# Kernel optimization log

Measured on AMD Instinct MI355X. Metric: run time of the kernel, lower is better.

## Reference

```python
import jax, jax.numpy as jnp
import numpy as np

NEG_POS_RATIO = 3
LOC_LOSS_ALPHA = 1.0
B, N, C = 64, 8732, 21  # batch, total prior boxes (SSD300), classes (VOC)


def setup_inputs() -> dict:
    key = jax.random.key(0)
    kd, km, kl, kpd, kpl = jax.random.split(key, 5)
    pos_mask = jax.random.bernoulli(km, 0.02, (B, N))
    actual_bbox_deltas = jax.random.normal(kd, (B, N, 4), dtype=jnp.float32) * pos_mask[..., None]
    cls = jax.random.randint(kl, (B, N), 0, C)
    actual_labels = jax.nn.one_hot(cls, C, dtype=jnp.float32)
    pred_bbox_deltas = jax.random.normal(kpd, (B, N, 4), dtype=jnp.float32)
    pred_labels = jax.random.normal(kpl, (B, N, C), dtype=jnp.float32)
    return {
        "actual_bbox_deltas": actual_bbox_deltas,
        "actual_labels": actual_labels,
        "pred_bbox_deltas": pred_bbox_deltas,
        "pred_labels": pred_labels,
    }


def reference(actual_bbox_deltas, actual_labels, pred_bbox_deltas, pred_labels):
    # positive boxes: any nonzero delta
    pos_cond = jnp.any(actual_bbox_deltas != 0, axis=2)          # [B, N] bool
    pos_count = jnp.sum(pos_cond, axis=1)                         # [B]
    neg_count = pos_count * NEG_POS_RATIO                         # [B]

    # CE from logits, used only to rank negatives for hard-negative mining
    ce_logits = -jnp.sum(actual_labels * jax.nn.log_softmax(pred_labels, axis=-1), axis=-1)  # [B, N]
    masked_loss = jnp.where(pos_cond, -jnp.inf, ce_logits)
    # rank[b, n] = position of box n in descending sort of masked_loss[b]
    order = jnp.argsort(-masked_loss, axis=1)
    rank = jnp.argsort(order, axis=1)
    neg_mask = rank < neg_count[:, None]                          # hardest negatives
    sel_mask = pos_cond | neg_mask                                # boxes entering conf loss

    total_pos = jnp.maximum(jnp.sum(pos_count), 1).astype(jnp.float32)

    # Huber (delta=1): TF Huber takes mean over last axis, then reduction='sum'
    d = pred_bbox_deltas - actual_bbox_deltas
    ad = jnp.abs(d)
    hub = jnp.where(ad <= 1.0, 0.5 * d * d, ad - 0.5)             # [B, N, 4]
    loc_loss = jnp.sum(jnp.mean(hub, axis=-1) * pos_cond) * LOC_LOSS_ALPHA

    # conf loss: TF CategoricalCrossentropy with from_logits=False (as in the original code,
    # applied to the raw pred_labels): normalize to sum 1, clip to epsilon, -sum(y*log p)
    eps = 1e-7
    p = pred_labels / jnp.sum(pred_labels, axis=-1, keepdims=True)
    p = jnp.clip(p, eps, 1.0 - eps)
    ce_probs = -jnp.sum(actual_labels * jnp.log(p), axis=-1)      # [B, N]
    conf_loss = jnp.sum(ce_probs * sel_mask)

    return loc_loss / total_pos, conf_loss / total_pos
```

## Files before the change

### kernel.cpp

```cpp
#include <hip/hip_runtime.h>
#include <math.h>

#define BB 64
#define NN 8732
#define NV4 (NN / 4)
#define CC 21
#define TB 128
#define GX 69
#define NIT 6

typedef unsigned int u32;
typedef __attribute__((address_space(1))) const u32 gu32;
typedef __attribute__((address_space(3))) u32 lu32;

static __device__ __forceinline__ unsigned f2u(float f) {
  unsigned u = __float_as_uint(f);
  return (u & 0x80000000u) ? ~u : (u | 0x80000000u);
}

__global__ __launch_bounds__(128) void k1_map(
    const float* __restrict__ abd, const float* __restrict__ lbl,
    const float* __restrict__ pbd, const float* __restrict__ plog,
    unsigned* __restrict__ keys, float* __restrict__ cep,
    float* __restrict__ pl, float* __restrict__ pc, int* __restrict__ pcnt) {
  __shared__ __align__(16) float s_plog[TB * CC];
  __shared__ int s_cls[TB];
  __shared__ float s_l[2], s_p[2];
  __shared__ int s_c[2];

  const int b = blockIdx.y;
  const int base = blockIdx.x * TB;
  const int nbox = min(TB, NN - base);
  const int nf4 = (nbox * CC) >> 2;
  const int tid = threadIdx.x;
  const int lane = tid & 63, wv = tid >> 6;

  const float4* pl4 = reinterpret_cast<const float4*>(plog + ((size_t)b * NN + base) * CC);
#pragma unroll
  for (int it = 0; it < NIT; ++it) {
    const int t = it * TB + tid;
    if (t < nf4) {
      __builtin_amdgcn_global_load_lds(
          (gu32*)(const u32*)(pl4 + t),
          (lu32*)(u32*)((char*)s_plog + (size_t)(it * TB + (tid & 64)) * 16),
          16, 0, 0);
    }
  }

  const float4* lb4 = reinterpret_cast<const float4*>(lbl + ((size_t)b * NN + base) * CC);
  float4 lv4[NIT];
#pragma unroll
  for (int it = 0; it < NIT; ++it) {
    const int t = it * TB + tid;
    lv4[it] = lb4[(t < nf4) ? t : 0];
  }
  const int nclamp = base + ((tid < nbox) ? tid : 0);
  const size_t idxc = (size_t)b * NN + nclamp;
  const float4 a = reinterpret_cast<const float4*>(abd)[idxc];
  const float4 p = reinterpret_cast<const float4*>(pbd)[idxc];

#pragma unroll
  for (int it = 0; it < NIT; ++it) {
    const int t = it * TB + tid;
    if (t < nf4) {
      const float4 v = lv4[it];
      const int f0 = t * 4;
      int box = f0 / CC;
      int rem = f0 - box * CC;
      if (v.x != 0.f) s_cls[box] = rem;
      if (++rem == CC) { rem = 0; ++box; }
      if (v.y != 0.f) s_cls[box] = rem;
      if (++rem == CC) { rem = 0; ++box; }
      if (v.z != 0.f) s_cls[box] = rem;
      if (++rem == CC) { rem = 0; ++box; }
      if (v.w != 0.f) s_cls[box] = rem;
    }
  }
  __syncthreads();

  const bool valid = (tid < nbox);
  float loc = 0.f, pconf = 0.f;
  int isPos = 0;
  if (valid) {
    const size_t idx = (size_t)b * NN + base + tid;
    isPos = (a.x != 0.f) || (a.y != 0.f) || (a.z != 0.f) || (a.w != 0.f);

    const int cls = s_cls[tid];
    float pv[CC];
    float m = -INFINITY, ssum = 0.f, tdot = 0.f;
#pragma unroll
    for (int j = 0; j < CC; ++j) {
      const float v = s_plog[tid * CC + j];
      pv[j] = v;
      m = fmaxf(m, v);
      ssum += v;
      tdot = (j == cls) ? v : tdot;
    }
    float es = 0.f;
#pragma unroll
    for (int j = 0; j < CC; ++j) es += expf(pv[j] - m);
    float pt = tdot / ssum;
    float ptc = fminf(fmaxf(pt, 1e-7f), 1.0f - 1e-7f);
    float cp = -logf(ptc);
    float cel = (m + logf(es)) - tdot;
    keys[idx] = isPos ? 0u : f2u(cel);
    cep[idx] = cp;
    pconf = isPos ? cp : 0.f;
    float dx = p.x - a.x, dy = p.y - a.y, dz = p.z - a.z, dw = p.w - a.w;
    float axv = fabsf(dx), ayv = fabsf(dy), azv = fabsf(dz), awv = fabsf(dw);
    float h = (axv <= 1.f ? 0.5f * dx * dx : axv - 0.5f)
            + (ayv <= 1.f ? 0.5f * dy * dy : ayv - 0.5f)
            + (azv <= 1.f ? 0.5f * dz * dz : azv - 0.5f)
            + (awv <= 1.f ? 0.5f * dw * dw : awv - 0.5f);
    loc = isPos ? h * 0.25f : 0.f;
  }
  float lvv = loc, pcf = pconf;
  int pctr = isPos;
  for (int off = 32; off > 0; off >>= 1) {
    lvv += __shfl_down(lvv, off, 64);
    pcf += __shfl_down(pcf, off, 64);
    pctr += __shfl_down(pctr, off, 64);
  }
  if (lane == 0) { s_l[wv] = lvv; s_p[wv] = pcf; s_c[wv] = pctr; }
  __syncthreads();
  if (tid == 0) {
    const int bi = b * GX + blockIdx.x;
    pl[bi] = s_l[0] + s_l[1];
    pc[bi] = s_p[0] + s_p[1];
    pcnt[bi] = s_c[0] + s_c[1];
  }
}

#define K2T 1024
#define K2W 16

__global__ __launch_bounds__(K2T) void k2_select(
    const unsigned* __restrict__ keys, const float* __restrict__ cep,
    const float* __restrict__ pl, const float* __restrict__ pc,
    const int* __restrict__ pcnt,
    double* __restrict__ row_loc, double* __restrict__ row_conf,
    int* __restrict__ row_pos) {
  __shared__ unsigned hist[2048];
  __shared__ unsigned wsum[K2W];
  __shared__ unsigned bc[2];
  __shared__ unsigned wtot[K2W];
  __shared__ double s_d[K2W];
  __shared__ double s_rl, s_rc;
  __shared__ int s_pos;
  const int b = blockIdx.x;
  const int tid = threadIdx.x;
  const int lane = tid & 63, wv = tid >> 6;

  if (wv == 0) {
    float a = 0.f, c = 0.f;
    int p = 0;
    for (int i = lane; i < GX; i += 64) {
      a += pl[b * GX + i];
      c += pc[b * GX + i];
      p += pcnt[b * GX + i];
    }
    for (int off = 32; off > 0; off >>= 1) {
      a += __shfl_down(a, off, 64);
      c += __shfl_down(c, off, 64);
      p += __shfl_down(p, off, 64);
    }
    if (lane == 0) { s_rl = (double)a; s_rc = (double)c; s_pos = p; }
  }
  __syncthreads();
  const int pos = s_pos;
  unsigned k = (unsigned)(pos * 3);
  const unsigned negs = (unsigned)(NN - pos);
  if (k > negs) k = negs;

  double neg_total = 0.0;
  if (k > 0) {
    const unsigned* rk = keys + (size_t)b * NN;
    const uint4* rk4 = reinterpret_cast<const uint4*>(rk);
    unsigned want = k;
    unsigned prefix = 0;
    for (int pass = 0; pass < 3; ++pass) {
      const int nb = (pass == 2) ? 1024 : 2048;
      const int shift = (pass == 0) ? 21 : (pass == 1) ? 10 : 0;
      for (int i = tid; i < nb; i += K2T) hist[i] = 0;
      __syncthreads();
      if (pass == 0) {
        for (int t = tid; t < NV4; t += K2T) {
          uint4 v = rk4[t];
          atomicAdd(&hist[v.x >> 21], 1u);
          atomicAdd(&hist[v.y >> 21], 1u);
          atomicAdd(&hist[v.z >> 21], 1u);
          atomicAdd(&hist[v.w >> 21], 1u);
        }
      } else {
        const unsigned pshift = (pass == 1) ? 21u : 10u;
        const unsigned msk = (unsigned)(nb - 1);
        for (int t = tid; t < NV4; t += K2T) {
          uint4 v = rk4[t];
          if ((v.x >> pshift) == prefix) atomicAdd(&hist[(v.x >> shift) & msk], 1u);
          if ((v.y >> pshift) == prefix) atomicAdd(&hist[(v.y >> shift) & msk], 1u);
          if ((v.z >> pshift) == prefix) atomicAdd(&hist[(v.z >> shift) & msk], 1u);
          if ((v.w >> pshift) == prefix) atomicAdd(&hist[(v.w >> shift) & msk], 1u);
        }
      }
      __syncthreads();
      const int PR = nb / K2T;
      unsigned v0, v1 = 0, ls;
      if (PR == 2) {
        v0 = hist[nb - 1 - (tid * 2)];
        v1 = hist[nb - 1 - (tid * 2 + 1)];
        ls = v0 + v1;
      } else {
        v0 = hist[nb - 1 - tid];
        ls = v0;
      }
      unsigned x = ls;
#pragma unroll
      for (int off = 1; off < 64; off <<= 1) {
        unsigned y = __shfl_up(x, off, 64);
        if (lane >= off) x += y;
      }
      if (lane == 63) wsum[wv] = x;
      __syncthreads();
      if (wv == 0 && lane < K2W) {
        unsigned wx = wsum[lane];
#pragma unroll
        for (int off = 1; off < K2W; off <<= 1) {
          unsigned wy = __shfl_up(wx, off, K2W);
          if ((lane & (K2W - 1)) >= off) wx += wy;
        }
        wsum[lane] = wx;
      }
      __syncthreads();
      const unsigned woff = (wv == 0) ? 0u : wsum[wv - 1];
      const unsigned pinc = woff + x;
      if (PR == 2) {
        const unsigned p0 = pinc - ls + v0;
        const unsigned p1 = pinc;
        if (v0 > 0 && p0 >= want && p0 - v0 < want) { bc[0] = (unsigned)(nb - 1 - tid * 2); bc[1] = want - (p0 - v0); }
        if (v1 > 0 && p1 >= want && p1 - v1 < want) { bc[0] = (unsigned)(nb - 1 - (tid * 2 + 1)); bc[1] = want - (p1 - v1); }
      } else {
        if (v0 > 0 && pinc >= want && pinc - v0 < want) { bc[0] = (unsigned)(nb - 1 - tid); bc[1] = want - (pinc - v0); }
      }
      __syncthreads();
      const unsigned d = bc[0];
      want = bc[1];
      prefix = (pass == 0) ? d : ((prefix << ((pass == 1) ? 11 : 10)) | d);
      __syncthreads();
    }
    const unsigned tau = prefix;
    const unsigned neq = want;

    const float* rc = cep + (size_t)b * NN;
    double mysum = 0.0;
    unsigned bbase = 0;
    for (int start = 0; start < NN; start += K2T) {
      const int i = start + tid;
      const unsigned key = (i < NN) ? rk[i] : 0u;
      const bool gt = (i < NN) && (key > tau);
      const bool eq = (i < NN) && (key == tau);
      if (gt) mysum += (double)rc[i];
      const unsigned long long mb = __ballot(eq);
      if (lane == 0) wtot[wv] = (unsigned)__popcll(mb);
      __syncthreads();
      unsigned wpref = 0, tot = 0;
#pragma unroll
      for (int w = 0; w < K2W; ++w) {
        const unsigned c = wtot[w];
        wpref += (w < wv) ? c : 0u;
        tot += c;
      }
      if (eq) {
        const unsigned lanepref = (unsigned)__popcll(mb & ((1ull << lane) - 1ull));
        if (bbase + wpref + lanepref < neq) mysum += (double)rc[i];
      }
      bbase += tot;
      __syncthreads();
    }
    for (int off = 32; off > 0; off >>= 1) mysum += __shfl_down(mysum, off, 64);
    if (lane == 0) s_d[wv] = mysum;
    __syncthreads();
    if (tid == 0) {
#pragma unroll
      for (int w = 0; w < K2W; ++w) neg_total += s_d[w];
    }
  }
  if (tid == 0) {
    row_loc[b] = s_rl;
    row_conf[b] = s_rc + neg_total;
    row_pos[b] = pos;
  }
}

__global__ void k3_final(const double* __restrict__ row_loc,
                         const double* __restrict__ row_conf,
                         const int* __restrict__ row_pos,
                         float* __restrict__ out) {
  const int lane = threadIdx.x;
  double l = row_loc[lane], c = row_conf[lane];
  int p = row_pos[lane];
  for (int off = 32; off > 0; off >>= 1) {
    l += __shfl_down(l, off, 64);
    c += __shfl_down(c, off, 64);
    p += __shfl_down(p, off, 64);
  }
  if (lane == 0) {
    const double tot = (p > 0) ? (double)p : 1.0;
    out[0] = (float)(l / tot);
    out[1] = (float)(c / tot);
  }
}

extern "C" void kernel_launch(void* const* d_in, const int* in_sizes, int n_in,
                              void* d_out, int out_size, void* d_ws, size_t ws_size,
                              hipStream_t stream) {
  const float* abd = (const float*)d_in[0];
  const float* lbl = (const float*)d_in[1];
  const float* pbd = (const float*)d_in[2];
  const float* plog = (const float*)d_in[3];

  char* ws = (char*)d_ws;
  float* pl = (float*)(ws + 0);
  float* pc = (float*)(ws + 17920);
  int* pcnt = (int*)(ws + 35840);
  double* row_loc = (double*)(ws + 53760);
  double* row_conf = (double*)(ws + 54272);
  int* row_pos = (int*)(ws + 54784);
  unsigned* keys = (unsigned*)(ws + 55040);
  float* cep = (float*)(ws + 55040 + (size_t)BB * NN * sizeof(unsigned));

  dim3 g1(GX, BB);
  k1_map<<<g1, TB, 0, stream>>>(abd, lbl, pbd, plog, keys, cep, pl, pc, pcnt);
  k2_select<<<BB, K2T, 0, stream>>>(keys, cep, pl, pc, pcnt, row_loc, row_conf, row_pos);
  k3_final<<<1, 64, 0, stream>>>(row_loc, row_conf, row_pos, (float*)d_out);
}
```

Before: 43.18 us.

## Make k1 persistent over five tiles with register double-buffered prefetch

The map kernel now has each block process five consecutive 128-box tiles. Global loads of the next tiles go into registers while the current tile is computed, and shared memory is double-buffered with explicit barriers. This replaces the one-tile-per-block grid that used global_load_lds. It aims to hide load latency and cut the number of blocks and partial sums. The cost is far fewer blocks (14x64 instead of 69x64), which reduces parallelism on a large GPU, plus higher register pressure from the prefetch buffers.

```diff
diff --git a/kernel.cpp b/kernel.cpp
--- a/kernel.cpp
+++ b/kernel.cpp
@@ -6,12 +6,9 @@
 #define NV4 (NN / 4)
 #define CC 21
 #define TB 128
-#define GX 69
-#define NIT 6
-
-typedef unsigned int u32;
-typedef __attribute__((address_space(1))) const u32 gu32;
-typedef __attribute__((address_space(3))) u32 lu32;
+#define TPB 5
+#define NT 69
+#define GXB 14
 
 static __device__ __forceinline__ unsigned f2u(float f) {
   unsigned u = __float_as_uint(f);
@@ -23,74 +20,77 @@
     const float* __restrict__ pbd, const float* __restrict__ plog,
     unsigned* __restrict__ keys, float* __restrict__ cep,
     float* __restrict__ pl, float* __restrict__ pc, int* __restrict__ pcnt) {
-  __shared__ __align__(16) float s_plog[TB * CC];
-  __shared__ int s_cls[TB];
+  __shared__ __align__(16) float s_plog[2][TB * CC];
+  __shared__ int s_cls[2][TB];
   __shared__ float s_l[2], s_p[2];
   __shared__ int s_c[2];
 
   const int b = blockIdx.y;
-  const int base = blockIdx.x * TB;
-  const int nbox = min(TB, NN - base);
-  const int nf4 = (nbox * CC) >> 2;
+  const int bx = blockIdx.x;
   const int tid = threadIdx.x;
   const int lane = tid & 63, wv = tid >> 6;
-
-  const float4* pl4 = reinterpret_cast<const float4*>(plog + ((size_t)b * NN + base) * CC);
-#pragma unroll
-  for (int it = 0; it < NIT; ++it) {
-    const int t = it * TB + tid;
-    if (t < nf4) {
-      __builtin_amdgcn_global_load_lds(
-          (gu32*)(const u32*)(pl4 + t),
-          (lu32*)(u32*)((char*)s_plog + (size_t)(it * TB + (tid & 64)) * 16),
-          16, 0, 0);
-    }
-  }
-
-  const float4* lb4 = reinterpret_cast<const float4*>(lbl + ((size_t)b * NN + base) * CC);
-  float4 lv4[NIT];
-#pragma unroll
-  for (int it = 0; it < NIT; ++it) {
-    const int t = it * TB + tid;
-    lv4[it] = lb4[(t < nf4) ? t : 0];
-  }
-  const int nclamp = base + ((tid < nbox) ? tid : 0);
-  const size_t idxc = (size_t)b * NN + nclamp;
-  const float4 a = reinterpret_cast<const float4*>(abd)[idxc];
-  const float4 p = reinterpret_cast<const float4*>(pbd)[idxc];
-
-#pragma unroll
-  for (int it = 0; it < NIT; ++it) {
-    const int t = it * TB + tid;
-    if (t < nf4) {
-      const float4 v = lv4[it];
-      const int f0 = t * 4;
-      int box = f0 / CC;
-      int rem = f0 - box * CC;
-      if (v.x != 0.f) s_cls[box] = rem;
-      if (++rem == CC) { rem = 0; ++box; }
-      if (v.y != 0.f) s_cls[box] = rem;
-      if (++rem == CC) { rem = 0; ++box; }
-      if (v.z != 0.f) s_cls[box] = rem;
-      if (++rem == CC) { rem = 0; ++box; }
-      if (v.w != 0.f) s_cls[box] = rem;
-    }
-  }
-  __syncthreads();
-
-  const bool valid = (tid < nbox);
-  float loc = 0.f, pconf = 0.f;
-  int isPos = 0;
-  if (valid) {
-    const size_t idx = (size_t)b * NN + base + tid;
-    isPos = (a.x != 0.f) || (a.y != 0.f) || (a.z != 0.f) || (a.w != 0.f);
-
-    const int cls = s_cls[tid];
+  const size_t rowbase = (size_t)b * NN;
+  const float4* plog4 = reinterpret_cast<const float4*>(plog + rowbase * CC);
+  const float4* lbl4 = reinterpret_cast<const float4*>(lbl + rowbase * CC);
+  const float4* abd4 = reinterpret_cast<const float4*>(abd);
+  const float4* pbd4 = reinterpret_cast<const float4*>(pbd);
+
+  float4 Lp[2][6], Ll[2][6], Ab[2], Pb[2];
+  float th_loc = 0.f, th_conf = 0.f;
+  int th_cnt = 0;
+
+  auto LOADT = [&](int s, int tt) {
+    const int ttc = (tt > NT - 1) ? (NT - 1) : tt;
+    const int nbox = min(TB, NN - ttc * TB);
+    const int nf4 = (nbox * CC) >> 2;
+    const int base4 = ttc * ((TB * CC) >> 2);
+#pragma unroll
+    for (int it = 0; it < 6; ++it) {
+      int t4 = it * TB + tid;
+      t4 = (t4 < nf4) ? t4 : (nf4 - 1);
+      Lp[s][it] = plog4[base4 + t4];
+      Ll[s][it] = lbl4[base4 + t4];
+    }
+    const int n = ttc * TB + ((tid < nbox) ? tid : (nbox - 1));
+    Ab[s] = abd4[rowbase + n];
+    Pb[s] = pbd4[rowbase + n];
+  };
+
+  auto STAGE = [&](int s, int u, int tt) {
+    const int nbox = min(TB, NN - tt * TB);
+    const int nf4 = (nbox * CC) >> 2;
+#pragma unroll
+    for (int it = 0; it < 6; ++it) {
+      const int t4 = it * TB + tid;
+      if (t4 < nf4) {
+        reinterpret_cast<float4*>(s_plog[u])[t4] = Lp[s][it];
+        const float4 v = Ll[s][it];
+        const int f0 = t4 * 4;
+        int box = f0 / CC;
+        int rem = f0 - box * CC;
+        if (v.x != 0.f) s_cls[u][box] = rem;
+        if (++rem == CC) { rem = 0; ++box; }
+        if (v.y != 0.f) s_cls[u][box] = rem;
+        if (++rem == CC) { rem = 0; ++box; }
+        if (v.z != 0.f) s_cls[u][box] = rem;
+        if (++rem == CC) { rem = 0; ++box; }
+        if (v.w != 0.f) s_cls[u][box] = rem;
+      }
+    }
+  };
+
+  auto COMPUTE = [&](int s, int u, int tt) {
+    const int nbox = min(TB, NN - tt * TB);
+    if (tid >= nbox) return;
+    const size_t idx = rowbase + tt * TB + tid;
+    const float4 a = Ab[s], p = Pb[s];
+    const int isPos = (a.x != 0.f) || (a.y != 0.f) || (a.z != 0.f) || (a.w != 0.f);
+    const int cls = s_cls[u][tid];
     float pv[CC];
     float m = -INFINITY, ssum = 0.f, tdot = 0.f;
 #pragma unroll
     for (int j = 0; j < CC; ++j) {
-      const float v = s_plog[tid * CC + j];
+      const float v = s_plog[u][tid * CC + j];
       pv[j] = v;
       m = fmaxf(m, v);
       ssum += v;
@@ -99,23 +99,52 @@
     float es = 0.f;
 #pragma unroll
     for (int j = 0; j < CC; ++j) es += expf(pv[j] - m);
-    float pt = tdot / ssum;
-    float ptc = fminf(fmaxf(pt, 1e-7f), 1.0f - 1e-7f);
-    float cp = -logf(ptc);
-    float cel = (m + logf(es)) - tdot;
+    const float pt = tdot / ssum;
+    const float ptc = fminf(fmaxf(pt, 1e-7f), 1.0f - 1e-7f);
+    const float cp = -logf(ptc);
+    const float cel = (m + logf(es)) - tdot;
     keys[idx] = isPos ? 0u : f2u(cel);
     cep[idx] = cp;
-    pconf = isPos ? cp : 0.f;
-    float dx = p.x - a.x, dy = p.y - a.y, dz = p.z - a.z, dw = p.w - a.w;
-    float axv = fabsf(dx), ayv = fabsf(dy), azv = fabsf(dz), awv = fabsf(dw);
-    float h = (axv <= 1.f ? 0.5f * dx * dx : axv - 0.5f)
-            + (ayv <= 1.f ? 0.5f * dy * dy : ayv - 0.5f)
-            + (azv <= 1.f ? 0.5f * dz * dz : azv - 0.5f)
-            + (awv <= 1.f ? 0.5f * dw * dw : awv - 0.5f);
-    loc = isPos ? h * 0.25f : 0.f;
-  }
-  float lvv = loc, pcf = pconf;
-  int pctr = isPos;
+    const float dx = p.x - a.x, dy = p.y - a.y, dz = p.z - a.z, dw = p.w - a.w;
+    const float axv = fabsf(dx), ayv = fabsf(dy), azv = fabsf(dz), awv = fabsf(dw);
+    const float h = (axv <= 1.f ? 0.5f * dx * dx : axv - 0.5f)
+                  + (ayv <= 1.f ? 0.5f * dy * dy : ayv - 0.5f)
+                  + (azv <= 1.f ? 0.5f * dz * dz : azv - 0.5f)
+                  + (awv <= 1.f ? 0.5f * dw * dw : awv - 0.5f);
+    if (isPos) {
+      th_loc += h * 0.25f;
+      th_conf += cp;
+      th_cnt += 1;
+    }
+  };
+
+  LOADT(0, bx * TPB + 0);
+  LOADT(1, bx * TPB + 1);
+  __builtin_amdgcn_sched_barrier(0);
+  STAGE(0, 0, bx * TPB + 0);
+  asm volatile("s_waitcnt lgkmcnt(0)" ::: "memory");
+  __builtin_amdgcn_sched_barrier(0);
+  __builtin_amdgcn_s_barrier();
+  __builtin_amdgcn_sched_barrier(0);
+
+#pragma unroll
+  for (int t = 0; t < TPB; ++t) {
+    if (t + 2 < TPB) LOADT(t & 1, bx * TPB + t + 2);
+    __builtin_amdgcn_sched_barrier(0);
+    const int tt = bx * TPB + t;
+    if (tt < NT) COMPUTE(t & 1, t & 1, tt);
+    if (t + 1 < TPB) {
+      const int tn = tt + 1;
+      if (tn < NT) STAGE((t + 1) & 1, (t + 1) & 1, tn);
+      asm volatile("s_waitcnt lgkmcnt(0)" ::: "memory");
+      __builtin_amdgcn_sched_barrier(0);
+      __builtin_amdgcn_s_barrier();
+      __builtin_amdgcn_sched_barrier(0);
+    }
+  }
+
+  float lvv = th_loc, pcf = th_conf;
+  int pctr = th_cnt;
   for (int off = 32; off > 0; off >>= 1) {
     lvv += __shfl_down(lvv, off, 64);
     pcf += __shfl_down(pcf, off, 64);
@@ -124,7 +153,7 @@
   if (lane == 0) { s_l[wv] = lvv; s_p[wv] = pcf; s_c[wv] = pctr; }
   __syncthreads();
   if (tid == 0) {
-    const int bi = b * GX + blockIdx.x;
+    const int bi = b * GXB + bx;
     pl[bi] = s_l[0] + s_l[1];
     pc[bi] = s_p[0] + s_p[1];
     pcnt[bi] = s_c[0] + s_c[1];
@@ -133,6 +162,7 @@
 
 #define K2T 1024
 #define K2W 16
+#define GX GXB
 
 __global__ __launch_bounds__(K2T) void k2_select(
     const unsigned* __restrict__ keys, const float* __restrict__ cep,
@@ -320,15 +350,15 @@
 
   char* ws = (char*)d_ws;
   float* pl = (float*)(ws + 0);
-  float* pc = (float*)(ws + 17920);
-  int* pcnt = (int*)(ws + 35840);
-  double* row_loc = (double*)(ws + 53760);
-  double* row_conf = (double*)(ws + 54272);
-  int* row_pos = (int*)(ws + 54784);
-  unsigned* keys = (unsigned*)(ws + 55040);
-  float* cep = (float*)(ws + 55040 + (size_t)BB * NN * sizeof(unsigned));
-
-  dim3 g1(GX, BB);
+  float* pc = (float*)(ws + 8960);
+  int* pcnt = (int*)(ws + 17920);
+  double* row_loc = (double*)(ws + 26880);
+  double* row_conf = (double*)(ws + 27392);
+  int* row_pos = (int*)(ws + 27904);
+  unsigned* keys = (unsigned*)(ws + 28160);
+  float* cep = (float*)(ws + 28160 + (size_t)BB * NN * sizeof(unsigned));
+
+  dim3 g1(GXB, BB);
   k1_map<<<g1, TB, 0, stream>>>(abd, lbl, pbd, plog, keys, cep, pl, pc, pcnt);
   k2_select<<<BB, K2T, 0, stream>>>(keys, cep, pl, pc, pcnt, row_loc, row_conf, row_pos);
   k3_final<<<1, 64, 0, stream>>>(row_loc, row_conf, row_pos, (float*)d_out);
```

Result: slower. 62.43 us (+44.6%).

## Stage all k1 inputs into LDS via async global_load_lds with 64-thread blocks

Applied to the files above, without the earlier changes.

The map kernel shrinks to single-wave 64-thread blocks (more blocks per row) and loads labels, box deltas and logits straight into LDS with global_load_lds, instead of register loads plus a scatter of class indices. The class index is now found by scanning the staged one-hot row in LDS, and the cross-wave shared-memory reduction and its extra barrier are dropped. This aims to cut register pressure and load latency and to raise occupancy, at the cost of more blocks, more partial sums for k2 and more LDS reads per thread.

```diff
diff --git a/kernel.cpp b/kernel.cpp
--- a/kernel.cpp
+++ b/kernel.cpp
@@ -5,9 +5,8 @@
 #define NN 8732
 #define NV4 (NN / 4)
 #define CC 21
-#define TB 128
-#define GX 69
-#define NIT 6
+#define TB 64
+#define GX 137
 
 typedef unsigned int u32;
 typedef __attribute__((address_space(1))) const u32 gu32;
@@ -18,74 +17,57 @@
   return (u & 0x80000000u) ? ~u : (u | 0x80000000u);
 }
 
-__global__ __launch_bounds__(128) void k1_map(
+#define GLDS(src, dstbase) \
+  __builtin_amdgcn_global_load_lds((gu32*)(const u32*)(src), (lu32*)(u32*)(dstbase), 16, 0, 0)
+
+__global__ __launch_bounds__(64) void k1_map(
     const float* __restrict__ abd, const float* __restrict__ lbl,
     const float* __restrict__ pbd, const float* __restrict__ plog,
     unsigned* __restrict__ keys, float* __restrict__ cep,
     float* __restrict__ pl, float* __restrict__ pc, int* __restrict__ pcnt) {
   __shared__ __align__(16) float s_plog[TB * CC];
-  __shared__ int s_cls[TB];
-  __shared__ float s_l[2], s_p[2];
-  __shared__ int s_c[2];
+  __shared__ __align__(16) float s_lbl[TB * CC];
+  __shared__ __align__(16) float4 s_ab[TB];
+  __shared__ __align__(16) float4 s_pb[TB];
 
   const int b = blockIdx.y;
   const int base = blockIdx.x * TB;
   const int nbox = min(TB, NN - base);
   const int nf4 = (nbox * CC) >> 2;
   const int tid = threadIdx.x;
-  const int lane = tid & 63, wv = tid >> 6;
-
-  const float4* pl4 = reinterpret_cast<const float4*>(plog + ((size_t)b * NN + base) * CC);
-#pragma unroll
-  for (int it = 0; it < NIT; ++it) {
+  const size_t rowbase = (size_t)b * NN;
+
+  const float4* plog4 = reinterpret_cast<const float4*>(plog + (rowbase + base) * CC);
+  const float4* lbl4 = reinterpret_cast<const float4*>(lbl + (rowbase + base) * CC);
+#pragma unroll
+  for (int it = 0; it < 6; ++it) {
     const int t = it * TB + tid;
     if (t < nf4) {
-      __builtin_amdgcn_global_load_lds(
-          (gu32*)(const u32*)(pl4 + t),
-          (lu32*)(u32*)((char*)s_plog + (size_t)(it * TB + (tid & 64)) * 16),
-          16, 0, 0);
-    }
-  }
-
-  const float4* lb4 = reinterpret_cast<const float4*>(lbl + ((size_t)b * NN + base) * CC);
-  float4 lv4[NIT];
-#pragma unroll
-  for (int it = 0; it < NIT; ++it) {
-    const int t = it * TB + tid;
-    lv4[it] = lb4[(t < nf4) ? t : 0];
-  }
-  const int nclamp = base + ((tid < nbox) ? tid : 0);
-  const size_t idxc = (size_t)b * NN + nclamp;
-  const float4 a = reinterpret_cast<const float4*>(abd)[idxc];
-  const float4 p = reinterpret_cast<const float4*>(pbd)[idxc];
-
-#pragma unroll
-  for (int it = 0; it < NIT; ++it) {
-    const int t = it * TB + tid;
-    if (t < nf4) {
-      const float4 v = lv4[it];
-      const int f0 = t * 4;
-      int box = f0 / CC;
-      int rem = f0 - box * CC;
-      if (v.x != 0.f) s_cls[box] = rem;
-      if (++rem == CC) { rem = 0; ++box; }
-      if (v.y != 0.f) s_cls[box] = rem;
-      if (++rem == CC) { rem = 0; ++box; }
-      if (v.z != 0.f) s_cls[box] = rem;
-      if (++rem == CC) { rem = 0; ++box; }
-      if (v.w != 0.f) s_cls[box] = rem;
-    }
-  }
+      GLDS(plog4 + t, (char*)s_plog + (size_t)it * TB * 16);
+      GLDS(lbl4 + t, (char*)s_lbl + (size_t)it * TB * 16);
+    }
+  }
+  if (tid < nbox) {
+    GLDS(reinterpret_cast<const float4*>(abd) + rowbase + base + tid, (char*)s_ab);
+    GLDS(reinterpret_cast<const float4*>(pbd) + rowbase + base + tid, (char*)s_pb);
+  }
+  asm volatile("s_waitcnt vmcnt(0)" ::: "memory");
+  __builtin_amdgcn_sched_barrier(0);
   __syncthreads();
 
-  const bool valid = (tid < nbox);
   float loc = 0.f, pconf = 0.f;
   int isPos = 0;
-  if (valid) {
-    const size_t idx = (size_t)b * NN + base + tid;
+  if (tid < nbox) {
+    const size_t idx = rowbase + base + tid;
+    const float4 a = s_ab[tid];
+    const float4 p = s_pb[tid];
     isPos = (a.x != 0.f) || (a.y != 0.f) || (a.z != 0.f) || (a.w != 0.f);
 
-    const int cls = s_cls[tid];
+    int cls = 0;
+#pragma unroll
+    for (int j = 0; j < CC; ++j)
+      cls = (s_lbl[tid * CC + j] != 0.f) ? j : cls;
+
     float pv[CC];
     float m = -INFINITY, ssum = 0.f, tdot = 0.f;
 #pragma unroll
@@ -99,19 +81,19 @@
     float es = 0.f;
 #pragma unroll
     for (int j = 0; j < CC; ++j) es += expf(pv[j] - m);
-    float pt = tdot / ssum;
-    float ptc = fminf(fmaxf(pt, 1e-7f), 1.0f - 1e-7f);
-    float cp = -logf(ptc);
-    float cel = (m + logf(es)) - tdot;
+    const float pt = tdot / ssum;
+    const float ptc = fminf(fmaxf(pt, 1e-7f), 1.0f - 1e-7f);
+    const float cp = -logf(ptc);
+    const float cel = (m + logf(es)) - tdot;
     keys[idx] = isPos ? 0u : f2u(cel);
     cep[idx] = cp;
     pconf = isPos ? cp : 0.f;
-    float dx = p.x - a.x, dy = p.y - a.y, dz = p.z - a.z, dw = p.w - a.w;
-    float axv = fabsf(dx), ayv = fabsf(dy), azv = fabsf(dz), awv = fabsf(dw);
-    float h = (axv <= 1.f ? 0.5f * dx * dx : axv - 0.5f)
-            + (ayv <= 1.f ? 0.5f * dy * dy : ayv - 0.5f)
-            + (azv <= 1.f ? 0.5f * dz * dz : azv - 0.5f)
-            + (awv <= 1.f ? 0.5f * dw * dw : awv - 0.5f);
+    const float dx = p.x - a.x, dy = p.y - a.y, dz = p.z - a.z, dw = p.w - a.w;
+    const float axv = fabsf(dx), ayv = fabsf(dy), azv = fabsf(dz), awv = fabsf(dw);
+    const float h = (axv <= 1.f ? 0.5f * dx * dx : axv - 0.5f)
+                  + (ayv <= 1.f ? 0.5f * dy * dy : ayv - 0.5f)
+                  + (azv <= 1.f ? 0.5f * dz * dz : azv - 0.5f)
+                  + (awv <= 1.f ? 0.5f * dw * dw : awv - 0.5f);
     loc = isPos ? h * 0.25f : 0.f;
   }
   float lvv = loc, pcf = pconf;
@@ -121,13 +103,11 @@
     pcf += __shfl_down(pcf, off, 64);
     pctr += __shfl_down(pctr, off, 64);
   }
-  if (lane == 0) { s_l[wv] = lvv; s_p[wv] = pcf; s_c[wv] = pctr; }
-  __syncthreads();
   if (tid == 0) {
     const int bi = b * GX + blockIdx.x;
-    pl[bi] = s_l[0] + s_l[1];
-    pc[bi] = s_p[0] + s_p[1];
-    pcnt[bi] = s_c[0] + s_c[1];
+    pl[bi] = lvv;
+    pc[bi] = pcf;
+    pcnt[bi] = pctr;
   }
 }
 
@@ -320,13 +300,13 @@
 
   char* ws = (char*)d_ws;
   float* pl = (float*)(ws + 0);
-  float* pc = (float*)(ws + 17920);
-  int* pcnt = (int*)(ws + 35840);
-  double* row_loc = (double*)(ws + 53760);
-  double* row_conf = (double*)(ws + 54272);
-  int* row_pos = (int*)(ws + 54784);
-  unsigned* keys = (unsigned*)(ws + 55040);
-  float* cep = (float*)(ws + 55040 + (size_t)BB * NN * sizeof(unsigned));
+  float* pc = (float*)(ws + 36864);
+  int* pcnt = (int*)(ws + 73728);
+  double* row_loc = (double*)(ws + 110592);
+  double* row_conf = (double*)(ws + 111104);
+  int* row_pos = (int*)(ws + 111616);
+  unsigned* keys = (unsigned*)(ws + 112128);
+  float* cep = (float*)(ws + 112128 + (size_t)BB * NN * sizeof(unsigned));
 
   dim3 g1(GX, BB);
   k1_map<<<g1, TB, 0, stream>>>(abd, lbl, pbd, plog, keys, cep, pl, pc, pcnt);
```

New measurement: 42.56 us. About the same (-1.4%).
